# Performance work log

Measured on AMD Instinct MI355X. Metric: run time of the kernel, lower is better.

Reference implementation:

```python
import jax, jax.numpy as jnp
import numpy as np

N = 50000      # total nodes (25 graphs x 2000 proteins)
E = 1200000    # total edges
G = 25         # graphs
F_IN = 128     # protein_features
H = 64         # hidden_dim
L = 2          # num_layers


def setup_inputs() -> dict:
    key = jax.random.key(0)
    ks = jax.random.split(key, 24)
    inp = {
        "x": jax.random.normal(ks[0], (N, F_IN), dtype=jnp.float32),
        "edge_attr": jax.random.uniform(ks[1], (E,), dtype=jnp.float32),
        "global_features": jax.random.normal(ks[2], (G, 6), dtype=jnp.float32),
        "edge_index": jax.random.randint(ks[3], (2, E), 0, N, dtype=jnp.int64),
        "batch": (jnp.arange(N, dtype=jnp.int64) // (N // G)),
    }
    s = 0.05
    inp["W_embed"] = jax.random.normal(ks[4], (F_IN, H), dtype=jnp.float32) * s
    inp["b_embed"] = jnp.zeros((H,), dtype=jnp.float32)
    inp["W_glob"] = jax.random.normal(ks[5], (6, H), dtype=jnp.float32) * s
    inp["b_glob"] = jnp.zeros((H,), dtype=jnp.float32)
    # stacked per-layer GATConv params (heads=1)
    inp["lin_W"] = jax.random.normal(ks[6], (L, H, H), dtype=jnp.float32) * s
    inp["att_src"] = jax.random.normal(ks[7], (L, H), dtype=jnp.float32) * s
    inp["att_dst"] = jax.random.normal(ks[8], (L, H), dtype=jnp.float32) * s
    inp["lin_edge_W"] = jax.random.normal(ks[9], (L, 1, H), dtype=jnp.float32) * s
    inp["att_edge"] = jax.random.normal(ks[10], (L, H), dtype=jnp.float32) * s
    inp["gat_bias"] = jnp.zeros((L, H), dtype=jnp.float32)
    inp["W_comb"] = jax.random.normal(ks[11], (2 * H, H), dtype=jnp.float32) * s
    inp["b_comb"] = jnp.zeros((H,), dtype=jnp.float32)
    inp["W_out"] = jax.random.normal(ks[12], (H, 1), dtype=jnp.float32) * s
    inp["b_out"] = jnp.zeros((1,), dtype=jnp.float32)
    return inp


def _forward(x, edge_attr, global_features, W_embed, b_embed, W_glob, b_glob,
             lin_W, att_src, att_dst, lin_edge_W, att_edge, gat_bias,
             W_comb, b_comb, W_out, b_out, edge_index, batch):
    src, dst = edge_index[0], edge_index[1]
    h = x @ W_embed + b_embed                       # [N,H]
    g = global_features @ W_glob + b_glob           # [G,H]
    ea = edge_attr[:, None]                         # [E,1] (edge_attr.unsqueeze(1))
    for l in range(L):
        hs = h @ lin_W[l]                           # [N,H] shared lin_src/lin_dst
        a_src = hs @ att_src[l]                     # [N]
        a_dst = hs @ att_dst[l]                     # [N]
        ef = ea @ lin_edge_W[l]                     # [E,H]
        a_edge = ef @ att_edge[l]                   # [E]
        alpha = jax.nn.leaky_relu(a_src[src] + a_dst[dst] + a_edge, 0.2)
        # segment softmax over incoming edges of each dst node
        m = jax.ops.segment_max(alpha, dst, num_segments=N)
        ex = jnp.exp(alpha - m[dst])
        denom = jax.ops.segment_sum(ex, dst, num_segments=N)
        alpha = ex / (denom[dst] + 1e-16)
        msg = alpha[:, None] * hs[src]              # [E,H]
        h = jax.ops.segment_sum(msg, dst, num_segments=N) + gat_bias[l]
        h = jax.nn.relu(h)
    # global_mean_pool
    counts = jax.ops.segment_sum(jnp.ones((N,), h.dtype), batch, num_segments=G)
    graph = jax.ops.segment_sum(h, batch, num_segments=G) / counts[:, None]
    combined = jax.nn.relu(jnp.concatenate([graph, g], axis=1) @ W_comb + b_comb)
    return combined @ W_out + b_out                 # [G,1]


def reference(x, edge_attr, global_features, W_embed, b_embed, W_glob, b_glob,
              lin_W, att_src, att_dst, lin_edge_W, att_edge, gat_bias,
              W_comb, b_comb, W_out, b_out, edge_index, batch):
    return _forward(x, edge_attr, global_features, W_embed, b_embed, W_glob, b_glob,
                    lin_W, att_src, att_dst, lin_edge_W, att_edge, gat_bias,
                    W_comb, b_comb, W_out, b_out, edge_index, batch)
```

## Files before the change

### kernel.cpp

```cpp
#include <hip/hip_runtime.h>
#include <hip/hip_fp16.h>
#include <math.h>

#define N_NODES 50000
#define N_EDGES 1200000
#define N_GRAPH 25
#define F_IN 128
#define H_DIM 64
#define NODES_PER_GRAPH 2000
#define POOL_CHUNKS 32

#define NBUCK 196
#define BUCK_CAP 8000
#define EPB 4096
#define NB_BIN ((N_EDGES + EPB - 1) / EPB)
#define NB_GEMM ((N_NODES + 63) / 64)

#define OFF_H     0
#define OFF_HS    (N_NODES*64)
#define OFF_ASRC  (OFF_HS + N_NODES*64)
#define OFF_ADST  (OFF_ASRC + N_NODES)
#define OFF_CBUF  (OFF_ADST + N_NODES)
#define OFF_BCUR  (OFF_CBUF + 16)
#define OFF_GSUM  (OFF_BCUR + 256)
#define OFF_ROWP  (OFF_GSUM + N_GRAPH*64)
#define OFF_ESRT  (OFF_ROWP + N_NODES + 2)
#define OFF_EL2   (OFF_ESRT + N_EDGES)

__global__ __launch_bounds__(256) void k_embed(const float* __restrict__ x,
                                               const float* __restrict__ W,
                                               const float* __restrict__ b,
                                               float* __restrict__ h,
                                               const float* __restrict__ linE,
                                               const float* __restrict__ attE,
                                               float* __restrict__ cbuf,
                                               int* __restrict__ bcur,
                                               float* __restrict__ gsum) {
    __shared__ float4 sW4[F_IN * 16];
    __shared__ float4 sx4[64 * 17];
    int tid = threadIdx.x;
    if (blockIdx.x == 0) {
        for (int i = tid; i < 256; i += 256) bcur[i] = 0;
        for (int i = tid; i < N_GRAPH * 64; i += 256) gsum[i] = 0.f;
        if (tid < 128) {
            int l = tid >> 6, j = tid & 63;
            float v = linE[l * 64 + j] * attE[l * 64 + j];
            #pragma unroll
            for (int m = 1; m < 64; m <<= 1) v += __shfl_xor(v, m);
            if (j == 0) cbuf[l] = v;
        }
    }
    int n0 = blockIdx.x * 64;
    const float4* W4 = (const float4*)W;
    const float4* x4 = (const float4*)x;
    #pragma unroll
    for (int i = 0; i < 8; ++i) sW4[tid + i * 256] = W4[tid + i * 256];

    int c4 = tid & 15, ng = tid >> 4;
    int r = tid >> 4, q = tid & 15;
    float4 acc[4];
    #pragma unroll
    for (int j = 0; j < 4; ++j) acc[j] = make_float4(0.f, 0.f, 0.f, 0.f);

    for (int kh = 0; kh < 2; ++kh) {
        __syncthreads();
        #pragma unroll
        for (int rb = 0; rb < 4; ++rb) {
            int rr = r + rb * 16;
            int n = n0 + rr;
            float4 v = make_float4(0.f, 0.f, 0.f, 0.f);
            if (n < N_NODES) v = x4[(size_t)n * 32 + kh * 16 + q];
            sx4[rr * 17 + q] = v;
        }
        __syncthreads();
        #pragma unroll
        for (int kq = 0; kq < 16; ++kq) {
            float4 wv[4];
            #pragma unroll
            for (int kk = 0; kk < 4; ++kk) wv[kk] = sW4[(kh * 64 + kq * 4 + kk) * 16 + c4];
            #pragma unroll
            for (int j = 0; j < 4; ++j) {
                float4 xv = sx4[(ng * 4 + j) * 17 + kq];
                float xs[4] = {xv.x, xv.y, xv.z, xv.w};
                #pragma unroll
                for (int kk = 0; kk < 4; ++kk) {
                    acc[j].x = fmaf(xs[kk], wv[kk].x, acc[j].x);
                    acc[j].y = fmaf(xs[kk], wv[kk].y, acc[j].y);
                    acc[j].z = fmaf(xs[kk], wv[kk].z, acc[j].z);
                    acc[j].w = fmaf(xs[kk], wv[kk].w, acc[j].w);
                }
            }
        }
    }
    float4 bb = ((const float4*)b)[c4];
    #pragma unroll
    for (int j = 0; j < 4; ++j) {
        int n = n0 + ng * 4 + j;
        if (n < N_NODES) {
            float4 v;
            v.x = acc[j].x + bb.x; v.y = acc[j].y + bb.y;
            v.z = acc[j].z + bb.z; v.w = acc[j].w + bb.w;
            ((float4*)h)[(size_t)n * 16 + c4] = v;
        }
    }
}

__global__ __launch_bounds__(256) void k_hs(const float* __restrict__ hin,
                                            const float* __restrict__ W,
                                            const float* __restrict__ attS,
                                            const float* __restrict__ attD,
                                            __half* __restrict__ hs_h,
                                            float* __restrict__ asrc,
                                            float* __restrict__ adst) {
    __shared__ float4 sW4[H_DIM * 16];
    __shared__ float4 sx4[64 * 17];
    int tid = threadIdx.x;
    int n0 = blockIdx.x * 64;
    const float4* W4 = (const float4*)W;
    const float4* h4 = (const float4*)hin;
    #pragma unroll
    for (int i = 0; i < 4; ++i) sW4[tid + i * 256] = W4[tid + i * 256];
    int r = tid >> 4, q = tid & 15;
    #pragma unroll
    for (int rb = 0; rb < 4; ++rb) {
        int rr = r + rb * 16;
        int n = n0 + rr;
        float4 v = make_float4(0.f, 0.f, 0.f, 0.f);
        if (n < N_NODES) v = h4[(size_t)n * 16 + q];
        sx4[rr * 17 + q] = v;
    }
    __syncthreads();

    int c4 = tid & 15, ng = tid >> 4;
    float4 acc[4];
    #pragma unroll
    for (int j = 0; j < 4; ++j) acc[j] = make_float4(0.f, 0.f, 0.f, 0.f);
    #pragma unroll
    for (int kq = 0; kq < 16; ++kq) {
        float4 wv[4];
        #pragma unroll
        for (int kk = 0; kk < 4; ++kk) wv[kk] = sW4[(kq * 4 + kk) * 16 + c4];
        #pragma unroll
        for (int j = 0; j < 4; ++j) {
            float4 xv = sx4[(ng * 4 + j) * 17 + kq];
            float xs[4] = {xv.x, xv.y, xv.z, xv.w};
            #pragma unroll
            for (int kk = 0; kk < 4; ++kk) {
                acc[j].x = fmaf(xs[kk], wv[kk].x, acc[j].x);
                acc[j].y = fmaf(xs[kk], wv[kk].y, acc[j].y);
                acc[j].z = fmaf(xs[kk], wv[kk].z, acc[j].z);
                acc[j].w = fmaf(xs[kk], wv[kk].w, acc[j].w);
            }
        }
    }
    float4 aS = ((const float4*)attS)[c4];
    float4 aD = ((const float4*)attD)[c4];
    #pragma unroll
    for (int j = 0; j < 4; ++j) {
        int n = n0 + ng * 4 + j;
        float rs = acc[j].x * aS.x + acc[j].y * aS.y + acc[j].z * aS.z + acc[j].w * aS.w;
        float rd = acc[j].x * aD.x + acc[j].y * aD.y + acc[j].z * aD.z + acc[j].w * aD.w;
        #pragma unroll
        for (int o = 1; o < 16; o <<= 1) {
            rs += __shfl_xor(rs, o);
            rd += __shfl_xor(rd, o);
        }
        if (n < N_NODES) {
            __half2 p0 = __floats2half2_rn(acc[j].x, acc[j].y);
            __half2 p1 = __floats2half2_rn(acc[j].z, acc[j].w);
            uint2 st;
            st.x = *(unsigned*)&p0;
            st.y = *(unsigned*)&p1;
            ((uint2*)hs_h)[(size_t)n * 16 + c4] = st;
            if (c4 == 0) { asrc[n] = rs; adst[n] = rd; }
        }
    }
}

__global__ __launch_bounds__(256) void k_el(const unsigned* __restrict__ esrt,
                                            const float* __restrict__ asrc,
                                            const float* __restrict__ cbuf,
                                            int layer,
                                            uint2* __restrict__ el2) {
    int e = blockIdx.x * 256 + threadIdx.x;
    if (e >= N_EDGES) return;
    unsigned v = esrt[e];
    unsigned s = v & 0xFFFFu;
    float eav = __uint_as_float(v & 0xFFFF0000u);
    float lg = asrc[s] + cbuf[layer] * eav;
    uint2 r; r.x = __float_as_uint(lg); r.y = s;
    el2[e] = r;
}

__device__ __forceinline__ int block_excl_scan(int v, int tid, int* lds, int* total) {
    int lane = tid & 63, w = tid >> 6;
    int incl = v;
    #pragma unroll
    for (int off = 1; off < 64; off <<= 1) {
        int t = __shfl_up(incl, off);
        if (lane >= off) incl += t;
    }
    if (lane == 63) lds[w] = incl;
    __syncthreads();
    int wo = 0;
    for (int i = 0; i < w; ++i) wo += lds[i];
    *total = lds[0] + lds[1] + lds[2] + lds[3];
    __syncthreads();
    return wo + incl - v;
}

__global__ __launch_bounds__(256) void k_bin(const int* __restrict__ ei,
                                             const float* __restrict__ ea,
                                             uint2* __restrict__ stage,
                                             int* __restrict__ bcur) {
    __shared__ int lcnt[NBUCK];
    __shared__ int lbase[NBUCK];
    int tid = threadIdx.x;
    for (int i = tid; i < NBUCK; i += 256) lcnt[i] = 0;
    __syncthreads();
    int e0 = blockIdx.x * EPB;
    unsigned pw0[16], pw1[16];
    #pragma unroll
    for (int k = 0; k < 16; ++k) {
        int e = e0 + k * 256 + tid;
        bool ok = e < N_EDGES;
        int s = ok ? ei[e] : 0;
        int d = ok ? ei[N_EDGES + e] : 0;
        float v = ok ? ea[e] : 0.f;
        pw0[k] = (unsigned)s | ((unsigned)d << 16);
        pw1[k] = __float_as_uint(v);
        if (ok) atomicAdd(&lcnt[d >> 8], 1);
    }
    __syncthreads();
    for (int i = tid; i < NBUCK; i += 256) {
        lbase[i] = atomicAdd(&bcur[i], lcnt[i]);
        lcnt[i] = 0;
    }
    __syncthreads();
    #pragma unroll
    for (int k = 0; k < 16; ++k) {
        int e = e0 + k * 256 + tid;
        if (e < N_EDGES) {
            int b = pw0[k] >> 24;
            int pos = lbase[b] + atomicAdd(&lcnt[b], 1);
            uint2 t; t.x = pw0[k]; t.y = pw1[k];
            stage[b * BUCK_CAP + pos] = t;
        }
    }
}

__global__ __launch_bounds__(256) void k_group(const uint2* __restrict__ stage,
                                               const int* __restrict__ bcur,
                                               int* __restrict__ rowp,
                                               unsigned* __restrict__ esrt) {
    int b = blockIdx.x;
    int tid = threadIdx.x;
    __shared__ int sprefix[256];
    __shared__ int lcnt[256];
    __shared__ int lofs[256];
    __shared__ int slds[4];
    int bv = (tid < NBUCK) ? bcur[tid] : 0;
    int total;
    int bex = block_excl_scan(bv, tid, slds, &total);
    sprefix[tid] = bex;
    lcnt[tid] = 0;
    __syncthreads();
    int base = sprefix[b];
    int cntb = bcur[b];
    const uint2* reg = stage + b * BUCK_CAP;
    for (int i = tid; i < cntb; i += 256)
        atomicAdd(&lcnt[(reg[i].x >> 16) & 255], 1);
    __syncthreads();
    int ex = block_excl_scan(lcnt[tid], tid, slds, &total);
    lofs[tid] = base + ex;
    int n = b * 256 + tid;
    if (n < N_NODES) rowp[n] = base + ex;
    if (b == 0 && tid == 0) rowp[N_NODES] = N_EDGES;
    __syncthreads();
    lcnt[tid] = 0;
    __syncthreads();
    for (int i = tid; i < cntb; i += 256) {
        uint2 v = reg[i];
        int dloc = (v.x >> 16) & 255;
        int pos = lofs[dloc] + atomicAdd(&lcnt[dloc], 1);
        esrt[pos] = (v.x & 0xFFFFu) | ((v.y + 0x8000u) & 0xFFFF0000u);
    }
}

__global__ __launch_bounds__(256) void k_fused(const int* __restrict__ rowp,
                                               const uint2* __restrict__ el2,
                                               const float* __restrict__ adst,
                                               const __half* __restrict__ hs_h,
                                               int layer,
                                               const float* __restrict__ gbias,
                                               float* __restrict__ hout) {
    int pair = (blockIdx.x * 256 + threadIdx.x) >> 6;
    int lane = threadIdx.x & 63;
    int half = lane >> 5, l32 = lane & 31;
    int wid = pair * 2 + half;
    if (wid >= N_NODES) return;
    int beg = rowp[wid], end = rowp[wid + 1];
    float adv = adst[wid];
    float m = -INFINITY, sum = 0.f;
    float acc[8];
    #pragma unroll
    for (int j = 0; j < 8; ++j) acc[j] = 0.f;
    int g = (lane >> 3) & 3;
    int fl8 = lane & 7;
    int hb = half * 32;
    const uint4* hsq = (const uint4*)hs_h;

#define UNPACK_FMA(w_, r_)                                                      \
    {                                                                           \
        __half2 h0_ = *(__half2*)&r_.x, h1_ = *(__half2*)&r_.y;                 \
        __half2 h2_ = *(__half2*)&r_.z, h3_ = *(__half2*)&r_.w;                 \
        float2 f0_ = __half22float2(h0_), f1_ = __half22float2(h1_);            \
        float2 f2_ = __half22float2(h2_), f3_ = __half22float2(h3_);            \
        acc[0] = fmaf(w_, f0_.x, acc[0]); acc[1] = fmaf(w_, f0_.y, acc[1]);     \
        acc[2] = fmaf(w_, f1_.x, acc[2]); acc[3] = fmaf(w_, f1_.y, acc[3]);     \
        acc[4] = fmaf(w_, f2_.x, acc[4]); acc[5] = fmaf(w_, f2_.y, acc[5]);     \
        acc[6] = fmaf(w_, f3_.x, acc[6]); acc[7] = fmaf(w_, f3_.y, acc[7]);     \
    }

    for (int base = beg; base < end; base += 32) {
        int idx = base + l32;
        bool ok = idx < end;
        float a;
        int s = 0;
        if (ok) {
            uint2 v = el2[idx];
            s = (int)v.y;
            a = __uint_as_float(v.x) + adv;
            a = a >= 0.f ? a : 0.2f * a;
        } else {
            a = -INFINITY;
        }
        float cm = a;
        #pragma unroll
        for (int o = 1; o < 32; o <<= 1) cm = fmaxf(cm, __shfl_xor(cm, o));
        float newm = fmaxf(m, cm);
        float scale = __expf(m - newm);
        sum *= scale;
        #pragma unroll
        for (int j = 0; j < 8; ++j) acc[j] *= scale;
        m = newm;
        float ex = ok ? __expf(a - m) : 0.f;
        float cs = ex;
        #pragma unroll
        for (int o = 1; o < 32; o <<= 1) cs += __shfl_xor(cs, o);
        sum += cs;

        int lim = end - base; if (lim > 32) lim = 32;
        int t = g;
        for (; t + 12 < lim; t += 16) {
            float w0 = __shfl(ex, hb + t),      w1 = __shfl(ex, hb + t + 4);
            float w2 = __shfl(ex, hb + t + 8),  w3 = __shfl(ex, hb + t + 12);
            int   s0 = __shfl(s, hb + t),       s1 = __shfl(s, hb + t + 4);
            int   s2 = __shfl(s, hb + t + 8),   s3 = __shfl(s, hb + t + 12);
            uint4 r0 = hsq[s0 * 8 + fl8];
            uint4 r1 = hsq[s1 * 8 + fl8];
            uint4 r2 = hsq[s2 * 8 + fl8];
            uint4 r3 = hsq[s3 * 8 + fl8];
            UNPACK_FMA(w0, r0);
            UNPACK_FMA(w1, r1);
            UNPACK_FMA(w2, r2);
            UNPACK_FMA(w3, r3);
        }
        for (; t < lim; t += 4) {
            float w0 = __shfl(ex, hb + t);
            int   s0 = __shfl(s, hb + t);
            uint4 r0 = hsq[s0 * 8 + fl8];
            UNPACK_FMA(w0, r0);
        }
    }
#undef UNPACK_FMA
    #pragma unroll
    for (int o = 8; o < 32; o <<= 1) {
        #pragma unroll
        for (int j = 0; j < 8; ++j) acc[j] += __shfl_xor(acc[j], o);
    }

    if (l32 < 8) {
        float inv = 1.f / (sum + 1e-16f);
        const float* gb = gbias + layer * H_DIM + l32 * 8;
        float* op = hout + (size_t)wid * H_DIM + l32 * 8;
        float4 v0, v1;
        v0.x = acc[0] * inv + gb[0]; v0.x = v0.x > 0.f ? v0.x : 0.f;
        v0.y = acc[1] * inv + gb[1]; v0.y = v0.y > 0.f ? v0.y : 0.f;
        v0.z = acc[2] * inv + gb[2]; v0.z = v0.z > 0.f ? v0.z : 0.f;
        v0.w = acc[3] * inv + gb[3]; v0.w = v0.w > 0.f ? v0.w : 0.f;
        v1.x = acc[4] * inv + gb[4]; v1.x = v1.x > 0.f ? v1.x : 0.f;
        v1.y = acc[5] * inv + gb[5]; v1.y = v1.y > 0.f ? v1.y : 0.f;
        v1.z = acc[6] * inv + gb[6]; v1.z = v1.z > 0.f ? v1.z : 0.f;
        v1.w = acc[7] * inv + gb[7]; v1.w = v1.w > 0.f ? v1.w : 0.f;
        ((float4*)op)[0] = v0;
        ((float4*)op)[1] = v1;
    }
}

__global__ __launch_bounds__(256) void k_pool(const float* __restrict__ h,
                                              float* __restrict__ gsum) {
    int g = blockIdx.x / POOL_CHUNKS;
    int chunk = blockIdx.x % POOL_CHUNKS;
    int wave = threadIdx.x >> 6, lane = threadIdx.x & 63;
    const int per_chunk = (NODES_PER_GRAPH + POOL_CHUNKS - 1) / POOL_CHUNKS;
    int n0 = g * NODES_PER_GRAPH + chunk * per_chunk;
    int n1 = g * NODES_PER_GRAPH + min((chunk + 1) * per_chunk, NODES_PER_GRAPH);
    float sum = 0.f;
    for (int n = n0 + wave; n < n1; n += 4)
        sum += h[(size_t)n * H_DIM + lane];
    __shared__ float spart[4][64];
    spart[wave][lane] = sum;
    __syncthreads();
    if (wave == 0) {
        float tot = spart[0][lane] + spart[1][lane] + spart[2][lane] + spart[3][lane];
        atomicAdd(gsum + g * H_DIM + lane, tot);
    }
}

__global__ __launch_bounds__(64) void k_head2(const float* __restrict__ gsum,
                                              const float* __restrict__ gf,
                                              const float* __restrict__ Wg,
                                              const float* __restrict__ bg,
                                              const float* __restrict__ Wc,
                                              const float* __restrict__ bc,
                                              const float* __restrict__ Wo,
                                              const float* __restrict__ bo,
                                              float* __restrict__ out) {
    int g = blockIdx.x;
    int lane = threadIdx.x;
    __shared__ float sgraph[64];
    __shared__ float sgf[64];
    sgraph[lane] = gsum[g * H_DIM + lane] / (float)NODES_PER_GRAPH;
    float gv = bg[lane];
    #pragma unroll
    for (int k = 0; k < 6; ++k) gv += gf[g * 6 + k] * Wg[k * 64 + lane];
    sgf[lane] = gv;
    __syncthreads();
    float cj = bc[lane];
    #pragma unroll
    for (int k = 0; k < 64; ++k) cj += sgraph[k] * Wc[k * 64 + lane];
    #pragma unroll
    for (int k = 0; k < 64; ++k) cj += sgf[k] * Wc[(64 + k) * 64 + lane];
    cj = cj > 0.f ? cj : 0.f;
    float o = cj * Wo[lane];
    #pragma unroll
    for (int m = 1; m < 64; m <<= 1) o += __shfl_xor(o, m);
    if (lane == 0) out[g] = o + bo[0];
}

extern "C" void kernel_launch(void* const* d_in, const int* in_sizes, int n_in,
                              void* d_out, int out_size, void* d_ws, size_t ws_size,
                              hipStream_t stream) {
    const float* x        = (const float*)d_in[0];
    const float* ea       = (const float*)d_in[1];
    const float* gf       = (const float*)d_in[2];
    const int*   ei       = (const int*)d_in[3];
    const float* W_embed  = (const float*)d_in[5];
    const float* b_embed  = (const float*)d_in[6];
    const float* W_glob   = (const float*)d_in[7];
    const float* b_glob   = (const float*)d_in[8];
    const float* lin_W    = (const float*)d_in[9];
    const float* att_src  = (const float*)d_in[10];
    const float* att_dst  = (const float*)d_in[11];
    const float* lin_eW   = (const float*)d_in[12];
    const float* att_edge = (const float*)d_in[13];
    const float* gat_bias = (const float*)d_in[14];
    const float* W_comb   = (const float*)d_in[15];
    const float* b_comb   = (const float*)d_in[16];
    const float* W_out    = (const float*)d_in[17];
    const float* b_out    = (const float*)d_in[18];
    float* out = (float*)d_out;
    float* ws  = (float*)d_ws;

    float*    h      = ws + OFF_H;
    __half*   hs_h   = (__half*)(ws + OFF_HS);
    uint2*    stage  = (uint2*)(ws + OFF_HS);
    float*    asrc   = ws + OFF_ASRC;
    float*    adst   = ws + OFF_ADST;
    float*    cbuf   = ws + OFF_CBUF;
    int*      bcur   = (int*)(ws + OFF_BCUR);
    float*    gsum   = ws + OFF_GSUM;
    int*      rowp   = (int*)(ws + OFF_ROWP);
    unsigned* esrt   = (unsigned*)(ws + OFF_ESRT);
    uint2*    el2    = (uint2*)(ws + OFF_EL2);

    k_embed<<<NB_GEMM, 256, 0, stream>>>(x, W_embed, b_embed, h,
                                         lin_eW, att_edge, cbuf, bcur, gsum);

    k_bin<<<NB_BIN, 256, 0, stream>>>(ei, ea, stage, bcur);
    k_group<<<NBUCK, 256, 0, stream>>>(stage, bcur, rowp, esrt);

    const int egrid = (N_EDGES + 255) / 256;
    const int fgrid = (N_NODES / 2 + 3) / 4;

    for (int l = 0; l < 2; ++l) {
        k_hs<<<NB_GEMM, 256, 0, stream>>>(h, lin_W + l * 64 * 64,
                                          att_src + l * 64, att_dst + l * 64,
                                          hs_h, asrc, adst);
        k_el<<<egrid, 256, 0, stream>>>(esrt, asrc, cbuf, l, el2);
        k_fused<<<fgrid, 256, 0, stream>>>(rowp, el2, adst, hs_h, l, gat_bias, h);
    }

    k_pool<<<N_GRAPH * POOL_CHUNKS, 256, 0, stream>>>(h, gsum);
    k_head2<<<N_GRAPH, 64, 0, stream>>>(gsum, gf, W_glob, b_glob,
                                        W_comb, b_comb, W_out, b_out, out);
}
```

Before: 192.8 us.

## Fuse layer-0 edge logits into grouping and drop online softmax max tracking

Moves the stage buffer to its own workspace region so the first k_hs can run before binning. k_group then writes the layer-0 edge logits (el2) directly, removing one k_el launch and its pass over the edges. In k_fused, the online-softmax running max with per-chunk rescaling is replaced by a plain exp-sum, normalised once at the end. This saves shuffles and rescale multiplies, but risks float overflow if attention logits become large, since no max is subtracted.

```diff
diff --git a/kernel.cpp b/kernel.cpp
--- a/kernel.cpp
+++ b/kernel.cpp
@@ -26,6 +26,7 @@
 #define OFF_ROWP  (OFF_GSUM + N_GRAPH*64)
 #define OFF_ESRT  (OFF_ROWP + N_NODES + 2)
 #define OFF_EL2   (OFF_ESRT + N_EDGES)
+#define OFF_STAGE (OFF_EL2 + 2*N_EDGES)
 
 __global__ __launch_bounds__(256) void k_embed(const float* __restrict__ x,
                                                const float* __restrict__ W,
@@ -252,7 +253,10 @@
 __global__ __launch_bounds__(256) void k_group(const uint2* __restrict__ stage,
                                                const int* __restrict__ bcur,
                                                int* __restrict__ rowp,
-                                               unsigned* __restrict__ esrt) {
+                                               unsigned* __restrict__ esrt,
+                                               const float* __restrict__ asrc,
+                                               const float* __restrict__ cbuf,
+                                               uint2* __restrict__ el2) {
     int b = blockIdx.x;
     int tid = threadIdx.x;
     __shared__ int sprefix[256];
@@ -267,6 +271,7 @@
     __syncthreads();
     int base = sprefix[b];
     int cntb = bcur[b];
+    float c0 = cbuf[0];
     const uint2* reg = stage + b * BUCK_CAP;
     for (int i = tid; i < cntb; i += 256)
         atomicAdd(&lcnt[(reg[i].x >> 16) & 255], 1);
@@ -283,7 +288,12 @@
         uint2 v = reg[i];
         int dloc = (v.x >> 16) & 255;
         int pos = lofs[dloc] + atomicAdd(&lcnt[dloc], 1);
-        esrt[pos] = (v.x & 0xFFFFu) | ((v.y + 0x8000u) & 0xFFFF0000u);
+        unsigned s = v.x & 0xFFFFu;
+        unsigned eab = (v.y + 0x8000u) & 0xFFFF0000u;
+        esrt[pos] = s | eab;
+        float lg = asrc[s] + c0 * __uint_as_float(eab);
+        uint2 r; r.x = __float_as_uint(lg); r.y = s;
+        el2[pos] = r;
     }
 }
 
@@ -301,7 +311,7 @@
     if (wid >= N_NODES) return;
     int beg = rowp[wid], end = rowp[wid + 1];
     float adv = adst[wid];
-    float m = -INFINITY, sum = 0.f;
+    float psum = 0.f;
     float acc[8];
     #pragma unroll
     for (int j = 0; j < 8; ++j) acc[j] = 0.f;
@@ -325,38 +335,24 @@
     for (int base = beg; base < end; base += 32) {
         int idx = base + l32;
         bool ok = idx < end;
-        float a;
+        float exv = 0.f;
         int s = 0;
         if (ok) {
             uint2 v = el2[idx];
             s = (int)v.y;
-            a = __uint_as_float(v.x) + adv;
+            float a = __uint_as_float(v.x) + adv;
             a = a >= 0.f ? a : 0.2f * a;
-        } else {
-            a = -INFINITY;
-        }
-        float cm = a;
-        #pragma unroll
-        for (int o = 1; o < 32; o <<= 1) cm = fmaxf(cm, __shfl_xor(cm, o));
-        float newm = fmaxf(m, cm);
-        float scale = __expf(m - newm);
-        sum *= scale;
-        #pragma unroll
-        for (int j = 0; j < 8; ++j) acc[j] *= scale;
-        m = newm;
-        float ex = ok ? __expf(a - m) : 0.f;
-        float cs = ex;
-        #pragma unroll
-        for (int o = 1; o < 32; o <<= 1) cs += __shfl_xor(cs, o);
-        sum += cs;
+            exv = __expf(a);
+        }
+        psum += exv;
 
         int lim = end - base; if (lim > 32) lim = 32;
         int t = g;
         for (; t + 12 < lim; t += 16) {
-            float w0 = __shfl(ex, hb + t),      w1 = __shfl(ex, hb + t + 4);
-            float w2 = __shfl(ex, hb + t + 8),  w3 = __shfl(ex, hb + t + 12);
-            int   s0 = __shfl(s, hb + t),       s1 = __shfl(s, hb + t + 4);
-            int   s2 = __shfl(s, hb + t + 8),   s3 = __shfl(s, hb + t + 12);
+            float w0 = __shfl(exv, hb + t),      w1 = __shfl(exv, hb + t + 4);
+            float w2 = __shfl(exv, hb + t + 8),  w3 = __shfl(exv, hb + t + 12);
+            int   s0 = __shfl(s, hb + t),        s1 = __shfl(s, hb + t + 4);
+            int   s2 = __shfl(s, hb + t + 8),    s3 = __shfl(s, hb + t + 12);
             uint4 r0 = hsq[s0 * 8 + fl8];
             uint4 r1 = hsq[s1 * 8 + fl8];
             uint4 r2 = hsq[s2 * 8 + fl8];
@@ -367,7 +363,7 @@
             UNPACK_FMA(w3, r3);
         }
         for (; t < lim; t += 4) {
-            float w0 = __shfl(ex, hb + t);
+            float w0 = __shfl(exv, hb + t);
             int   s0 = __shfl(s, hb + t);
             uint4 r0 = hsq[s0 * 8 + fl8];
             UNPACK_FMA(w0, r0);
@@ -375,13 +371,15 @@
     }
 #undef UNPACK_FMA
     #pragma unroll
+    for (int o = 1; o < 32; o <<= 1) psum += __shfl_xor(psum, o);
+    #pragma unroll
     for (int o = 8; o < 32; o <<= 1) {
         #pragma unroll
         for (int j = 0; j < 8; ++j) acc[j] += __shfl_xor(acc[j], o);
     }
 
     if (l32 < 8) {
-        float inv = 1.f / (sum + 1e-16f);
+        float inv = 1.f / (psum + 1e-16f);
         const float* gb = gbias + layer * H_DIM + l32 * 8;
         float* op = hout + (size_t)wid * H_DIM + l32 * 8;
         float4 v0, v1;
@@ -475,7 +473,6 @@
 
     float*    h      = ws + OFF_H;
     __half*   hs_h   = (__half*)(ws + OFF_HS);
-    uint2*    stage  = (uint2*)(ws + OFF_HS);
     float*    asrc   = ws + OFF_ASRC;
     float*    adst   = ws + OFF_ADST;
     float*    cbuf   = ws + OFF_CBUF;
@@ -484,23 +481,24 @@
     int*      rowp   = (int*)(ws + OFF_ROWP);
     unsigned* esrt   = (unsigned*)(ws + OFF_ESRT);
     uint2*    el2    = (uint2*)(ws + OFF_EL2);
+    uint2*    stage  = (uint2*)(ws + OFF_STAGE);
+
+    const int egrid = (N_EDGES + 255) / 256;
+    const int fgrid = (N_NODES / 2 + 3) / 4;
 
     k_embed<<<NB_GEMM, 256, 0, stream>>>(x, W_embed, b_embed, h,
                                          lin_eW, att_edge, cbuf, bcur, gsum);
+    k_hs<<<NB_GEMM, 256, 0, stream>>>(h, lin_W,
+                                      att_src, att_dst, hs_h, asrc, adst);
 
     k_bin<<<NB_BIN, 256, 0, stream>>>(ei, ea, stage, bcur);
-    k_group<<<NBUCK, 256, 0, stream>>>(stage, bcur, rowp, esrt);
-
-    const int egrid = (N_EDGES + 255) / 256;
-    const int fgrid = (N_NODES / 2 + 3) / 4;
-
-    for (int l = 0; l < 2; ++l) {
-        k_hs<<<NB_GEMM, 256, 0, stream>>>(h, lin_W + l * 64 * 64,
-                                          att_src + l * 64, att_dst + l * 64,
-                                          hs_h, asrc, adst);
-        k_el<<<egrid, 256, 0, stream>>>(esrt, asrc, cbuf, l, el2);
-        k_fused<<<fgrid, 256, 0, stream>>>(rowp, el2, adst, hs_h, l, gat_bias, h);
-    }
+    k_group<<<NBUCK, 256, 0, stream>>>(stage, bcur, rowp, esrt, asrc, cbuf, el2);
+
+    k_fused<<<fgrid, 256, 0, stream>>>(rowp, el2, adst, hs_h, 0, gat_bias, h);
+    k_hs<<<NB_GEMM, 256, 0, stream>>>(h, lin_W + 64 * 64,
+                                      att_src + 64, att_dst + 64, hs_h, asrc, adst);
+    k_el<<<egrid, 256, 0, stream>>>(esrt, asrc, cbuf, 1, el2);
+    k_fused<<<fgrid, 256, 0, stream>>>(rowp, el2, adst, hs_h, 1, gat_bias, h);
 
     k_pool<<<N_GRAPH * POOL_CHUNKS, 256, 0, stream>>>(h, gsum);
     k_head2<<<N_GRAPH, 64, 0, stream>>>(gsum, gf, W_glob, b_glob,
```

Result: faster. 187.6 us (-2.7%).
